# Performance work log

Measured on AMD Instinct MI355X. Metric: run time of the kernel, lower is better.

The kernel has to match this reference:

```python
import jax, jax.numpy as jnp
import numpy as np

MODEL_DIM = 512
KEY_DIM = 64


def setup_inputs() -> dict:
    key = jax.random.key(0)
    ks = jax.random.split(key, 8)
    B, S = 4, 4096
    scale = 1.0 / np.sqrt(MODEL_DIM)
    return {
        "x1": jax.random.normal(ks[0], (B, S, MODEL_DIM), jnp.float32),
        "x2": jax.random.normal(ks[1], (B, S, MODEL_DIM), jnp.float32),
        "Wq": jax.random.normal(ks[2], (MODEL_DIM, KEY_DIM), jnp.float32) * scale,
        "bq": jnp.zeros((KEY_DIM,), jnp.float32),
        "Wk": jax.random.normal(ks[3], (MODEL_DIM, KEY_DIM), jnp.float32) * scale,
        "bk": jnp.zeros((KEY_DIM,), jnp.float32),
        "Wv": jax.random.normal(ks[4], (MODEL_DIM, KEY_DIM), jnp.float32) * scale,
        "bv": jnp.zeros((KEY_DIM,), jnp.float32),
        "apply_mask": 1,
    }


def reference(x1, x2, Wq, bq, Wk, bk, Wv, bv, apply_mask):
    # Linear + ReLU projections (single head, d_k = d_v = KEY_DIM)
    q = jax.nn.relu(x1 @ Wq + bq)  # [B,S,dk]
    k = jax.nn.relu(x2 @ Wk + bk)  # [B,S,dk]
    v = jax.nn.relu(x2 @ Wv + bv)  # [B,S,dk]
    scores = jnp.einsum("bqd,bkd->bqk", q, k) / jnp.sqrt(jnp.float32(KEY_DIM))
    if apply_mask:
        S = scores.shape[-1]
        causal = jnp.tril(jnp.ones((S, S), dtype=bool))  # keep lower-tri incl. diag
        scores = jnp.where(causal, scores, -jnp.inf)
    attn = jax.nn.softmax(scores, axis=-1)
    return jnp.einsum("bqk,bkd->bqd", attn, v)
```

## Files before the change

### kernel.cpp

```cpp
#include <hip/hip_runtime.h>


typedef __attribute__((ext_vector_type(8))) _Float16 f16x8;
typedef __attribute__((ext_vector_type(4))) float f32x4;
typedef __attribute__((ext_vector_type(8))) unsigned short us8;

#define AS1 __attribute__((address_space(1)))
#define AS3 __attribute__((address_space(3)))

__device__ __forceinline__ void gload16(const void* g, void* l) {
  __builtin_amdgcn_global_load_lds((const AS1 unsigned int*)g,
                                   (AS3 unsigned int*)l, 16, 0, 0);
}

__device__ __forceinline__ unsigned short f2h(float f) {
  _Float16 h = (_Float16)f;
  return __builtin_bit_cast(unsigned short, h);
}
__device__ __forceinline__ float h2f(unsigned short u) {
  return (float)__builtin_bit_cast(_Float16, u);
}
__device__ __forceinline__ f16x8 us2h(us8 v) {
  return __builtin_bit_cast(f16x8, v);
}

#define S_LEN 4096
#define NROW 16384
#define CCH 8
#define NPMAX 8

__global__ __launch_bounds__(256) void prep_kernel(
    const float* __restrict__ Wq, const float* __restrict__ Wk,
    const float* __restrict__ Wv, unsigned short* __restrict__ wtT) {
  const int kc = blockIdx.x, p = blockIdx.y;
  const float* __restrict__ W = (p == 0) ? Wq : (p == 1) ? Wk : Wv;
  __shared__ unsigned short T[64][72];
  const int t = threadIdx.x;
#pragma unroll
  for (int i = 0; i < 4; i++) {
    int f = t + 256 * i;
    int kk = f >> 4, c4 = (f & 15) << 2;
    float4 v4 = *(const float4*)&W[(size_t)(kc * 64 + kk) * 64 + c4];
    T[c4 + 0][kk] = f2h(v4.x);
    T[c4 + 1][kk] = f2h(v4.y);
    T[c4 + 2][kk] = f2h(v4.z);
    T[c4 + 3][kk] = f2h(v4.w);
  }
  __syncthreads();
  const int n = t >> 2, q4 = (t & 3) << 4;
  us8 o0, o1;
#pragma unroll
  for (int e = 0; e < 8; e++) o0[e] = T[n][q4 + e];
#pragma unroll
  for (int e = 0; e < 8; e++) o1[e] = T[n][q4 + 8 + e];
  unsigned short* dst = &wtT[((size_t)p * 64 + n) * 512 + kc * 64 + q4];
  *(us8*)&dst[0] = o0;
  *(us8*)&dst[8] = o1;
}

__global__ __launch_bounds__(128) void proj_kernel(
    const float* __restrict__ x1, const float* __restrict__ x2,
    const unsigned short* __restrict__ wtT, const float* __restrict__ bq,
    const float* __restrict__ bk, const float* __restrict__ bv,
    unsigned short* __restrict__ qo, unsigned short* __restrict__ ko,
    unsigned short* __restrict__ vto) {
  const int kind = blockIdx.y;
  const float* __restrict__ X = kind ? x2 : x1;
  const int row0 = blockIdx.x * 32;

  __shared__ __align__(16) float XB[2][32 * 64];

  const int t = threadIdx.x, ln = t & 63, w = t >> 6, lm = ln & 15, lg = ln >> 4;

  f32x4 acc0[4], acc1[4];
#pragma unroll
  for (int nt = 0; nt < 4; nt++)
#pragma unroll
    for (int e = 0; e < 4; e++) { acc0[nt][e] = 0.0f; acc1[nt][e] = 0.0f; }

  const unsigned short* __restrict__ wt0 =
      wtT + (size_t)(kind ? 1 : 0) * 64 * 512;
  const unsigned short* __restrict__ wt1 = wtT + (size_t)2 * 64 * 512;

  auto STAGE = [&](int kc, int bi) {
#pragma unroll
    for (int cc = 0; cc < 4; cc++) {
      int c = 4 * w + cc;
      int r = 4 * c + (ln >> 4);
      int s = ln & 15;
      int sg = (s & 8) | ((s & 7) ^ (r & 7));
      gload16(&X[(size_t)(row0 + r) * 512 + kc * 64 + sg * 4],
              &XB[bi][c * 256]);
    }
  };

  STAGE(0, 0);
  for (int kc = 0; kc < 8; kc++) {
    const int bi = kc & 1;
    if (kc < 7) STAGE(kc + 1, bi ^ 1);
    us8 B0[8], B1[8];
#pragma unroll
    for (int nt = 0; nt < 4; nt++)
#pragma unroll
      for (int h = 0; h < 2; h++)
        B0[nt * 2 + h] = *(const us8*)&wt0[(size_t)(16 * nt + lm) * 512 +
                                           kc * 64 + 32 * h + 8 * lg];
    if (kind) {
#pragma unroll
      for (int nt = 0; nt < 4; nt++)
#pragma unroll
        for (int h = 0; h < 2; h++)
          B1[nt * 2 + h] = *(const us8*)&wt1[(size_t)(16 * nt + lm) * 512 +
                                             kc * 64 + 32 * h + 8 * lg];
    }
    if (kind) {
      if (kc < 7) asm volatile("s_waitcnt vmcnt(20)" ::: "memory");
      else        asm volatile("s_waitcnt vmcnt(16)" ::: "memory");
    } else {
      if (kc < 7) asm volatile("s_waitcnt vmcnt(12)" ::: "memory");
      else        asm volatile("s_waitcnt vmcnt(8)" ::: "memory");
    }
    __builtin_amdgcn_sched_barrier(0);
    __builtin_amdgcn_s_barrier();

    const int R = 16 * w + lm;
    f16x8 af[2];
#pragma unroll
    for (int g = 0; g < 2; g++) {
      int sl0 = 8 * g + ((2 * lg) ^ (lm & 7));
      int sl1 = 8 * g + ((2 * lg + 1) ^ (lm & 7));
      f32x4 a0 = *(const f32x4*)&XB[bi][R * 64 + sl0 * 4];
      f32x4 a1 = *(const f32x4*)&XB[bi][R * 64 + sl1 * 4];
      f16x8 v;
      v[0] = (_Float16)a0[0]; v[1] = (_Float16)a0[1];
      v[2] = (_Float16)a0[2]; v[3] = (_Float16)a0[3];
      v[4] = (_Float16)a1[0]; v[5] = (_Float16)a1[1];
      v[6] = (_Float16)a1[2]; v[7] = (_Float16)a1[3];
      af[g] = v;
    }
#pragma unroll
    for (int nt = 0; nt < 4; nt++) {
      acc0[nt] = __builtin_amdgcn_mfma_f32_16x16x32_f16(af[0], us2h(B0[nt * 2 + 0]), acc0[nt], 0, 0, 0);
      acc0[nt] = __builtin_amdgcn_mfma_f32_16x16x32_f16(af[1], us2h(B0[nt * 2 + 1]), acc0[nt], 0, 0, 0);
      if (kind) {
        acc1[nt] = __builtin_amdgcn_mfma_f32_16x16x32_f16(af[0], us2h(B1[nt * 2 + 0]), acc1[nt], 0, 0, 0);
        acc1[nt] = __builtin_amdgcn_mfma_f32_16x16x32_f16(af[1], us2h(B1[nt * 2 + 1]), acc1[nt], 0, 0, 0);
      }
    }
    __builtin_amdgcn_sched_barrier(0);
    __builtin_amdgcn_s_barrier();
  }

  if (kind == 0) {
#pragma unroll
    for (int nt = 0; nt < 4; nt++)
#pragma unroll
      for (int r = 0; r < 4; r++) {
        int row = row0 + 16 * w + 4 * lg + r;
        int col = 16 * nt + lm;
        float v = fmaxf(acc0[nt][r] + bq[col], 0.0f) * 0.125f;
        qo[(size_t)row * 64 + col] = f2h(v);
      }
  } else {
#pragma unroll
    for (int nt = 0; nt < 4; nt++)
#pragma unroll
      for (int r = 0; r < 4; r++) {
        int row = row0 + 16 * w + 4 * lg + r;
        int col = 16 * nt + lm;
        float v = fmaxf(acc0[nt][r] + bk[col], 0.0f);
        ko[(size_t)row * 64 + col] = f2h(v);
      }
    unsigned short* TB = (unsigned short*)&XB[0][0];
#pragma unroll
    for (int nt = 0; nt < 4; nt++)
#pragma unroll
      for (int r = 0; r < 4; r++) {
        float v = fmaxf(acc1[nt][r] + bv[16 * nt + lm], 0.0f);
        TB[(16 * w + 4 * lg + r) * 72 + 16 * nt + lm] = f2h(v);
      }
    __syncthreads();
    const int d = t >> 1, s0 = (t & 1) << 4;
    us8 o0, o1;
#pragma unroll
    for (int e = 0; e < 8; e++) o0[e] = TB[(s0 + e) * 72 + d];
#pragma unroll
    for (int e = 0; e < 8; e++) o1[e] = TB[(s0 + 8 + e) * 72 + d];
    const int batch = row0 >> 12, sl = row0 & 4095;
    unsigned short* vp = &vto[((size_t)batch * 64 + d) * S_LEN + sl + s0];
    *(us8*)&vp[0] = o0;
    *(us8*)&vp[8] = o1;
  }
}

__global__ __launch_bounds__(256) void attn_part(
    const unsigned short* __restrict__ q, const unsigned short* __restrict__ k,
    const unsigned short* __restrict__ vT, const int* __restrict__ amask,
    unsigned short* __restrict__ pO, float* __restrict__ pml) {
  const int qt = blockIdx.x, j = blockIdx.y, b = blockIdx.z;
  const int mask = *amask;
  const int sb = j * CCH;
  if (mask && sb > qt) return;
  const int se0 = sb + CCH - 1;
  const int se = mask ? ((qt < se0) ? qt : se0) : se0;

  const int t = threadIdx.x, ln = t & 63, w = t >> 6, lm = ln & 15, lg = ln >> 4;

  __shared__ __align__(16) unsigned short KB[2][4096];
  __shared__ __align__(16) unsigned short VB[2][4096];
  __shared__ __align__(16) unsigned short Ps[4][16][72];

  const unsigned short* __restrict__ qb = q + (size_t)b * S_LEN * 64;
  const unsigned short* __restrict__ kb = k + (size_t)b * S_LEN * 64;
  const unsigned short* __restrict__ vb = vT + (size_t)b * 64 * S_LEN;

  const size_t qoff = (size_t)(qt * 64 + 16 * w + lm) * 64;
  f16x8 qf0 = *(const f16x8*)&qb[qoff + 8 * lg];
  f16x8 qf1 = *(const f16x8*)&qb[qoff + 32 + 8 * lg];

  const int rr = ln >> 3;
  const int sg = (ln & 7) ^ (rr & 7);
  auto STAGE = [&](int s, int bi) {
    const int kv0 = s * 64;
#pragma unroll
    for (int cc = 0; cc < 2; cc++) {
      int c = 2 * w + cc;
      int r = 8 * c + rr;
      gload16(&kb[(size_t)(kv0 + r) * 64 + sg * 8], &KB[bi][c * 512]);
      gload16(&vb[(size_t)r * S_LEN + kv0 + sg * 8], &VB[bi][c * 512]);
    }
  };

  f32x4 accO[4];
#pragma unroll
  for (int dt = 0; dt < 4; dt++)
#pragma unroll
    for (int e = 0; e < 4; e++) accO[dt][e] = 0.0f;
  float m[4], lsum[4];
#pragma unroll
  for (int r = 0; r < 4; r++) { m[r] = -1e30f; lsum[r] = 0.0f; }

  const int sx = lm & 7;
  STAGE(sb, 0);
  for (int s = sb; s <= se; s++) {
    const int bi = (s - sb) & 1;
    if (s < se) {
      STAGE(s + 1, bi ^ 1);
      asm volatile("s_waitcnt vmcnt(4)" ::: "memory");
    } else {
      asm volatile("s_waitcnt vmcnt(0)" ::: "memory");
    }
    __builtin_amdgcn_sched_barrier(0);
    __builtin_amdgcn_s_barrier();

    f32x4 sc[4];
#pragma unroll
    for (int nt = 0; nt < 4; nt++) {
#pragma unroll
      for (int e = 0; e < 4; e++) sc[nt][e] = 0.0f;
      const int R = 16 * nt + lm;
      f16x8 kf0 = *(const f16x8*)&KB[bi][R * 64 + (lg ^ sx) * 8];
      f16x8 kf1 = *(const f16x8*)&KB[bi][R * 64 + ((4 + lg) ^ sx) * 8];
      sc[nt] = __builtin_amdgcn_mfma_f32_16x16x32_f16(qf0, kf0, sc[nt], 0, 0, 0);
      sc[nt] = __builtin_amdgcn_mfma_f32_16x16x32_f16(qf1, kf1, sc[nt], 0, 0, 0);
    }

    if (mask && s == qt) {
#pragma unroll
      for (int nt = 0; nt < 4; nt++)
#pragma unroll
        for (int r = 0; r < 4; r++)
          if (16 * nt + lm > 16 * w + 4 * lg + r) sc[nt][r] = -1e30f;
    }

    float pv[4][4];
#pragma unroll
    for (int r = 0; r < 4; r++) {
      float mx = fmaxf(fmaxf(sc[0][r], sc[1][r]), fmaxf(sc[2][r], sc[3][r]));
      mx = fmaxf(mx, __shfl_xor(mx, 1));
      mx = fmaxf(mx, __shfl_xor(mx, 2));
      mx = fmaxf(mx, __shfl_xor(mx, 4));
      mx = fmaxf(mx, __shfl_xor(mx, 8));
      float mn = fmaxf(m[r], mx);
      float fs = __expf(m[r] - mn);
      m[r] = mn;
      float su = 0.0f;
#pragma unroll
      for (int nt = 0; nt < 4; nt++) {
        pv[nt][r] = __expf(sc[nt][r] - mn);
        su += pv[nt][r];
      }
      su += __shfl_xor(su, 1);
      su += __shfl_xor(su, 2);
      su += __shfl_xor(su, 4);
      su += __shfl_xor(su, 8);
      lsum[r] = lsum[r] * fs + su;
#pragma unroll
      for (int dt = 0; dt < 4; dt++) accO[dt][r] *= fs;
    }

#pragma unroll
    for (int nt = 0; nt < 4; nt++)
#pragma unroll
      for (int r = 0; r < 4; r++)
        Ps[w][4 * lg + r][16 * nt + lm] = f2h(pv[nt][r]);

    f16x8 pf0 = *(const f16x8*)&Ps[w][lm][8 * lg];
    f16x8 pf1 = *(const f16x8*)&Ps[w][lm][32 + 8 * lg];
#pragma unroll
    for (int dt = 0; dt < 4; dt++) {
      const int R = 16 * dt + lm;
      f16x8 vf0 = *(const f16x8*)&VB[bi][R * 64 + (lg ^ sx) * 8];
      f16x8 vf1 = *(const f16x8*)&VB[bi][R * 64 + ((4 + lg) ^ sx) * 8];
      accO[dt] = __builtin_amdgcn_mfma_f32_16x16x32_f16(pf0, vf0, accO[dt], 0, 0, 0);
      accO[dt] = __builtin_amdgcn_mfma_f32_16x16x32_f16(pf1, vf1, accO[dt], 0, 0, 0);
    }
    __builtin_amdgcn_sched_barrier(0);
    __builtin_amdgcn_s_barrier();
  }

  const size_t ub = (size_t)(b * 64 + qt) * NPMAX + j;
  unsigned short* __restrict__ Op = pO + ub * 4096;
#pragma unroll
  for (int dt = 0; dt < 4; dt++)
#pragma unroll
    for (int r = 0; r < 4; r++)
      Op[(16 * w + 4 * lg + r) * 64 + 16 * dt + lm] = f2h(accO[dt][r]);
  if (lm == 0) {
    float* __restrict__ mlp = pml + ub * 128;
#pragma unroll
    for (int r = 0; r < 4; r++) {
      int row = 16 * w + 4 * lg + r;
      mlp[row * 2 + 0] = m[r];
      mlp[row * 2 + 1] = lsum[r];
    }
  }
}

__global__ __launch_bounds__(256) void combine_kernel(
    const unsigned short* __restrict__ pO, const float* __restrict__ pml,
    const int* __restrict__ amask, float* __restrict__ out) {
  const int qt = blockIdx.x, b = blockIdx.y;
  const int mask = *amask;
  const int np = mask ? (qt / CCH + 1) : NPMAX;
  const int t = threadIdx.x;
  const int row = t >> 2, cq = (t & 3) << 4;
  const size_t base = (size_t)(b * 64 + qt) * NPMAX;

  float M = -1e30f;
  for (int jj = 0; jj < np; jj++)
    M = fmaxf(M, pml[(base + jj) * 128 + row * 2]);

  float L = 0.0f;
  float a[16];
#pragma unroll
  for (int e = 0; e < 16; e++) a[e] = 0.0f;
  for (int jj = 0; jj < np; jj++) {
    const float* mlp = &pml[(base + jj) * 128 + row * 2];
    float wj = __expf(mlp[0] - M);
    L += mlp[1] * wj;
    const unsigned short* Op = &pO[(base + jj) * 4096 + row * 64 + cq];
    us8 h0 = *(const us8*)&Op[0];
    us8 h1 = *(const us8*)&Op[8];
#pragma unroll
    for (int e = 0; e < 8; e++) a[e] += wj * h2f(h0[e]);
#pragma unroll
    for (int e = 0; e < 8; e++) a[8 + e] += wj * h2f(h1[e]);
  }
  const float inv = 1.0f / L;
  float* op = &out[((size_t)b * S_LEN + qt * 64 + row) * 64 + cq];
  f32x4 o;
#pragma unroll
  for (int v4 = 0; v4 < 4; v4++) {
#pragma unroll
    for (int e = 0; e < 4; e++) o[e] = a[v4 * 4 + e] * inv;
    *(f32x4*)&op[v4 * 4] = o;
  }
}

extern "C" void kernel_launch(void* const* d_in, const int* in_sizes, int n_in,
                              void* d_out, int out_size, void* d_ws, size_t ws_size,
                              hipStream_t stream) {
  const float* x1 = (const float*)d_in[0];
  const float* x2 = (const float*)d_in[1];
  const float* Wq = (const float*)d_in[2];
  const float* bq = (const float*)d_in[3];
  const float* Wk = (const float*)d_in[4];
  const float* bk = (const float*)d_in[5];
  const float* Wv = (const float*)d_in[6];
  const float* bv = (const float*)d_in[7];
  const int* amask = (const int*)d_in[8];

  unsigned short* qws = (unsigned short*)d_ws;
  unsigned short* kws = qws + (size_t)NROW * 64;
  unsigned short* vtws = kws + (size_t)NROW * 64;
  unsigned short* wtT = vtws + (size_t)NROW * 64;
  unsigned short* pO = wtT + (size_t)3 * 64 * 512;
  float* pml = (float*)(pO + (size_t)2048 * 4096);
  float* out = (float*)d_out;

  prep_kernel<<<dim3(8, 3), 256, 0, stream>>>(Wq, Wk, Wv, wtT);
  proj_kernel<<<dim3(512, 2), 128, 0, stream>>>(x1, x2, wtT, bq, bk, bv,
                                                qws, kws, vtws);
  attn_part<<<dim3(64, NPMAX, 4), 256, 0, stream>>>(qws, kws, vtws, amask,
                                                    pO, pml);
  combine_kernel<<<dim3(64, 4), 256, 0, stream>>>(pO, pml, amask, out);
}
```

Baseline: 179.5 us.

## Transpose attention MFMA operands so softmax rows sit per lane; widen combine grid

```diff
diff --git a/kernel.cpp b/kernel.cpp
--- a/kernel.cpp
+++ b/kernel.cpp
@@ -4,6 +4,7 @@
 typedef __attribute__((ext_vector_type(8))) _Float16 f16x8;
 typedef __attribute__((ext_vector_type(4))) float f32x4;
 typedef __attribute__((ext_vector_type(8))) unsigned short us8;
+typedef __attribute__((ext_vector_type(4))) unsigned short us4;
 
 #define AS1 __attribute__((address_space(1)))
 #define AS3 __attribute__((address_space(3)))
@@ -97,7 +98,6 @@
   STAGE(0, 0);
   for (int kc = 0; kc < 8; kc++) {
     const int bi = kc & 1;
-    if (kc < 7) STAGE(kc + 1, bi ^ 1);
     us8 B0[8], B1[8];
 #pragma unroll
     for (int nt = 0; nt < 4; nt++)
@@ -113,6 +113,7 @@
           B1[nt * 2 + h] = *(const us8*)&wt1[(size_t)(16 * nt + lm) * 512 +
                                              kc * 64 + 32 * h + 8 * lg];
     }
+    if (kc < 7) STAGE(kc + 1, bi ^ 1);
     if (kind) {
       if (kc < 7) asm volatile("s_waitcnt vmcnt(20)" ::: "memory");
       else        asm volatile("s_waitcnt vmcnt(16)" ::: "memory");
@@ -236,9 +237,7 @@
   for (int dt = 0; dt < 4; dt++)
 #pragma unroll
     for (int e = 0; e < 4; e++) accO[dt][e] = 0.0f;
-  float m[4], lsum[4];
-#pragma unroll
-  for (int r = 0; r < 4; r++) { m[r] = -1e30f; lsum[r] = 0.0f; }
+  float m0 = -1e30f, l0 = 0.0f;
 
   const int sx = lm & 7;
   STAGE(sb, 0);
@@ -261,8 +260,8 @@
       const int R = 16 * nt + lm;
       f16x8 kf0 = *(const f16x8*)&KB[bi][R * 64 + (lg ^ sx) * 8];
       f16x8 kf1 = *(const f16x8*)&KB[bi][R * 64 + ((4 + lg) ^ sx) * 8];
-      sc[nt] = __builtin_amdgcn_mfma_f32_16x16x32_f16(qf0, kf0, sc[nt], 0, 0, 0);
-      sc[nt] = __builtin_amdgcn_mfma_f32_16x16x32_f16(qf1, kf1, sc[nt], 0, 0, 0);
+      sc[nt] = __builtin_amdgcn_mfma_f32_16x16x32_f16(kf0, qf0, sc[nt], 0, 0, 0);
+      sc[nt] = __builtin_amdgcn_mfma_f32_16x16x32_f16(kf1, qf1, sc[nt], 0, 0, 0);
     }
 
     if (mask && s == qt) {
@@ -270,40 +269,44 @@
       for (int nt = 0; nt < 4; nt++)
 #pragma unroll
         for (int r = 0; r < 4; r++)
-          if (16 * nt + lm > 16 * w + 4 * lg + r) sc[nt][r] = -1e30f;
-    }
+          if (16 * nt + 4 * lg + r > 16 * w + lm) sc[nt][r] = -1e30f;
+    }
+
+    float mx = fmaxf(fmaxf(fmaxf(sc[0][0], sc[0][1]), fmaxf(sc[0][2], sc[0][3])),
+                     fmaxf(fmaxf(sc[1][0], sc[1][1]), fmaxf(sc[1][2], sc[1][3])));
+    float mx2 = fmaxf(fmaxf(fmaxf(sc[2][0], sc[2][1]), fmaxf(sc[2][2], sc[2][3])),
+                      fmaxf(fmaxf(sc[3][0], sc[3][1]), fmaxf(sc[3][2], sc[3][3])));
+    mx = fmaxf(mx, mx2);
+    mx = fmaxf(mx, __shfl_xor(mx, 16));
+    mx = fmaxf(mx, __shfl_xor(mx, 32));
+    const float mn = fmaxf(m0, mx);
+    const float fs = __expf(m0 - mn);
+    m0 = mn;
 
     float pv[4][4];
-#pragma unroll
-    for (int r = 0; r < 4; r++) {
-      float mx = fmaxf(fmaxf(sc[0][r], sc[1][r]), fmaxf(sc[2][r], sc[3][r]));
-      mx = fmaxf(mx, __shfl_xor(mx, 1));
-      mx = fmaxf(mx, __shfl_xor(mx, 2));
-      mx = fmaxf(mx, __shfl_xor(mx, 4));
-      mx = fmaxf(mx, __shfl_xor(mx, 8));
-      float mn = fmaxf(m[r], mx);
-      float fs = __expf(m[r] - mn);
-      m[r] = mn;
-      float su = 0.0f;
-#pragma unroll
-      for (int nt = 0; nt < 4; nt++) {
+    float su = 0.0f;
+#pragma unroll
+    for (int nt = 0; nt < 4; nt++)
+#pragma unroll
+      for (int r = 0; r < 4; r++) {
         pv[nt][r] = __expf(sc[nt][r] - mn);
         su += pv[nt][r];
       }
-      su += __shfl_xor(su, 1);
-      su += __shfl_xor(su, 2);
-      su += __shfl_xor(su, 4);
-      su += __shfl_xor(su, 8);
-      lsum[r] = lsum[r] * fs + su;
-#pragma unroll
-      for (int dt = 0; dt < 4; dt++) accO[dt][r] *= fs;
-    }
-
-#pragma unroll
-    for (int nt = 0; nt < 4; nt++)
-#pragma unroll
-      for (int r = 0; r < 4; r++)
-        Ps[w][4 * lg + r][16 * nt + lm] = f2h(pv[nt][r]);
+    su += __shfl_xor(su, 16);
+    su += __shfl_xor(su, 32);
+    l0 = l0 * fs + su;
+#pragma unroll
+    for (int dt = 0; dt < 4; dt++)
+#pragma unroll
+      for (int e = 0; e < 4; e++) accO[dt][e] *= fs;
+
+#pragma unroll
+    for (int nt = 0; nt < 4; nt++) {
+      us4 w4;
+#pragma unroll
+      for (int r = 0; r < 4; r++) w4[r] = f2h(pv[nt][r]);
+      *(us4*)&Ps[w][lm][16 * nt + 4 * lg] = w4;
+    }
 
     f16x8 pf0 = *(const f16x8*)&Ps[w][lm][8 * lg];
     f16x8 pf1 = *(const f16x8*)&Ps[w][lm][32 + 8 * lg];
@@ -312,8 +315,8 @@
       const int R = 16 * dt + lm;
       f16x8 vf0 = *(const f16x8*)&VB[bi][R * 64 + (lg ^ sx) * 8];
       f16x8 vf1 = *(const f16x8*)&VB[bi][R * 64 + ((4 + lg) ^ sx) * 8];
-      accO[dt] = __builtin_amdgcn_mfma_f32_16x16x32_f16(pf0, vf0, accO[dt], 0, 0, 0);
-      accO[dt] = __builtin_amdgcn_mfma_f32_16x16x32_f16(pf1, vf1, accO[dt], 0, 0, 0);
+      accO[dt] = __builtin_amdgcn_mfma_f32_16x16x32_f16(vf0, pf0, accO[dt], 0, 0, 0);
+      accO[dt] = __builtin_amdgcn_mfma_f32_16x16x32_f16(vf1, pf1, accO[dt], 0, 0, 0);
     }
     __builtin_amdgcn_sched_barrier(0);
     __builtin_amdgcn_s_barrier();
@@ -322,29 +325,27 @@
   const size_t ub = (size_t)(b * 64 + qt) * NPMAX + j;
   unsigned short* __restrict__ Op = pO + ub * 4096;
 #pragma unroll
-  for (int dt = 0; dt < 4; dt++)
-#pragma unroll
-    for (int r = 0; r < 4; r++)
-      Op[(16 * w + 4 * lg + r) * 64 + 16 * dt + lm] = f2h(accO[dt][r]);
-  if (lm == 0) {
+  for (int dt = 0; dt < 4; dt++) {
+    us4 o4;
+#pragma unroll
+    for (int r = 0; r < 4; r++) o4[r] = f2h(accO[dt][r]);
+    *(us4*)&Op[(16 * w + lm) * 64 + 16 * dt + 4 * lg] = o4;
+  }
+  if (lg == 0) {
     float* __restrict__ mlp = pml + ub * 128;
-#pragma unroll
-    for (int r = 0; r < 4; r++) {
-      int row = 16 * w + 4 * lg + r;
-      mlp[row * 2 + 0] = m[r];
-      mlp[row * 2 + 1] = lsum[r];
-    }
+    mlp[(16 * w + lm) * 2 + 0] = m0;
+    mlp[(16 * w + lm) * 2 + 1] = l0;
   }
 }
 
 __global__ __launch_bounds__(256) void combine_kernel(
     const unsigned short* __restrict__ pO, const float* __restrict__ pml,
     const int* __restrict__ amask, float* __restrict__ out) {
-  const int qt = blockIdx.x, b = blockIdx.y;
+  const int qt = blockIdx.x, cg = blockIdx.y, b = blockIdx.z;
   const int mask = *amask;
   const int np = mask ? (qt / CCH + 1) : NPMAX;
   const int t = threadIdx.x;
-  const int row = t >> 2, cq = (t & 3) << 4;
+  const int row = t >> 2, c = ((t & 3) << 2) + (cg << 4);
   const size_t base = (size_t)(b * 64 + qt) * NPMAX;
 
   float M = -1e30f;
@@ -352,30 +353,20 @@
     M = fmaxf(M, pml[(base + jj) * 128 + row * 2]);
 
   float L = 0.0f;
-  float a[16];
-#pragma unroll
-  for (int e = 0; e < 16; e++) a[e] = 0.0f;
+  float a[4] = {0.f, 0.f, 0.f, 0.f};
   for (int jj = 0; jj < np; jj++) {
     const float* mlp = &pml[(base + jj) * 128 + row * 2];
     float wj = __expf(mlp[0] - M);
     L += mlp[1] * wj;
-    const unsigned short* Op = &pO[(base + jj) * 4096 + row * 64 + cq];
-    us8 h0 = *(const us8*)&Op[0];
-    us8 h1 = *(const us8*)&Op[8];
-#pragma unroll
-    for (int e = 0; e < 8; e++) a[e] += wj * h2f(h0[e]);
-#pragma unroll
-    for (int e = 0; e < 8; e++) a[8 + e] += wj * h2f(h1[e]);
+    us4 h = *(const us4*)&pO[(base + jj) * 4096 + row * 64 + c];
+#pragma unroll
+    for (int e = 0; e < 4; e++) a[e] += wj * h2f(h[e]);
   }
   const float inv = 1.0f / L;
-  float* op = &out[((size_t)b * S_LEN + qt * 64 + row) * 64 + cq];
   f32x4 o;
 #pragma unroll
-  for (int v4 = 0; v4 < 4; v4++) {
-#pragma unroll
-    for (int e = 0; e < 4; e++) o[e] = a[v4 * 4 + e] * inv;
-    *(f32x4*)&op[v4 * 4] = o;
-  }
+  for (int e = 0; e < 4; e++) o[e] = a[e] * inv;
+  *(f32x4*)&out[((size_t)b * S_LEN + qt * 64 + row) * 64 + c] = o;
 }
 
 extern "C" void kernel_launch(void* const* d_in, const int* in_sizes, int n_in,
@@ -404,5 +395,5 @@
                                                 qws, kws, vtws);
   attn_part<<<dim3(64, NPMAX, 4), 256, 0, stream>>>(qws, kws, vtws, amask,
                                                     pO, pml);
-  combine_kernel<<<dim3(64, 4), 256, 0, stream>>>(pO, pml, amask, out);
-}
+  combine_kernel<<<dim3(64, 4, 4), 256, 0, stream>>>(pO, pml, amask, out);
+}
```

Measured after the change: 165.7 us. 1.08x faster.
